# Performance work log

Measured on AMD Instinct MI355X. Metric: run time of the kernel, lower is better.

## Reference

```python
import jax, jax.numpy as jnp
import numpy as np

B, S, D = 8, 2048, 512          # batch, seq_len, latent_doc_dim
E = 512                          # embedding_dim (== latent_doc_dim here by construction)
NUM_CATS, NUM_LABELS = 1024, 8192
EMB_SCALING = 1.0


def _norm_embed(m, scaling):
    # __init__ preprocessing: m -= m.mean(); m /= m.std() * scaling
    m = m - m.mean()
    return m / (m.std() * scaling)


def setup_inputs() -> dict:
    key = jax.random.key(0)
    k1, k2, k3, k4, k5, k6, k7 = jax.random.split(key, 7)
    K = jax.random.normal(k1, (B, S, D), dtype=jnp.float32)
    V = jax.random.normal(k2, (B, S, D), dtype=jnp.float32)
    code2cat_map = jax.random.randint(k3, (NUM_LABELS,), 0, NUM_CATS)
    # pretrained embedding matrices, normalized as in __init__
    Q1_w = _norm_embed(jax.random.normal(k4, (NUM_CATS, E), dtype=jnp.float32), EMB_SCALING)
    Q2_w = _norm_embed(jax.random.normal(k5, (NUM_LABELS, E), dtype=jnp.float32), EMB_SCALING)
    # Conv1d(kernel_size=1): weight [D_out=latent, D_in=embed], bias [latent]
    map_w = jax.random.normal(k6, (D, E), dtype=jnp.float32) / np.sqrt(E)
    map_b = jax.random.normal(k7, (D,), dtype=jnp.float32) * 0.01
    return {"K": K, "V": V, "code2cat_map": code2cat_map,
            "Q1_w": Q1_w, "Q2_w": Q2_w, "map_w": map_w, "map_b": map_b}


def reference(K, V, code2cat_map, Q1_w, Q2_w, map_w, map_b):
    # kernel-size-1 Conv1d mapping == affine projection of each row embedding
    Q1 = jnp.einsum('ce,de->cd', Q1_w, map_w) + map_b        # [num_cats, D]
    Q2 = jnp.einsum('le,de->ld', Q2_w, map_w) + map_b        # [num_labels, D]
    # level-1 attention (scale=False)
    E1 = jnp.einsum('cd,bsd->bcs', Q1, K)                    # [B, num_cats, S]
    A1 = jax.nn.softmax(E1, axis=-1)
    C1 = jnp.einsum('bcs,bsd->bcd', A1, V)                   # [B, num_cats, D]
    # inject level-1 context into level-2 queries via code->category gather-add
    Q2b = Q2[None, :, :] + C1[:, code2cat_map, :]            # [B, num_labels, D]
    # level-2 attention
    E2 = jnp.einsum('bld,bsd->bls', Q2b, K)                  # [B, num_labels, S]
    A2 = jax.nn.softmax(E2, axis=-1)
    C2 = jnp.einsum('bls,bsd->bld', A2, V)                   # [B, num_labels, D]
    return (C2, E2)
```

## Files before the change

kernel.cpp:

```cpp
#include <hip/hip_runtime.h>
#include <hip/hip_bf16.h>
#include <stdint.h>

#define BB 8
#define SS 2048
#define DD 512
#define NCAT 1024
#define NLAB 8192

typedef short bf16x8 __attribute__((ext_vector_type(8)));
typedef short bf16x4_t __attribute__((ext_vector_type(4)));
typedef float f32x4 __attribute__((ext_vector_type(4)));

#define BAR() do { asm volatile("" ::: "memory"); __builtin_amdgcn_s_barrier(); asm volatile("" ::: "memory"); } while (0)

__device__ __forceinline__ unsigned short f2bf(float f) {
  union { float f; unsigned int u; } v; v.f = f;
  unsigned int u = v.u;
  return (unsigned short)((u + 0x7fffu + ((u >> 16) & 1u)) >> 16);
}
__device__ __forceinline__ float bf2f(unsigned short h) {
  union { unsigned int u; float f; } v; v.u = ((unsigned int)h) << 16;
  return v.f;
}

__device__ __forceinline__ void gload_lds16(const void* g, void* l) {
  __builtin_amdgcn_global_load_lds(
      (const __attribute__((address_space(1))) unsigned int*)g,
      (__attribute__((address_space(3))) unsigned int*)l, 16, 0, 0);
}

__global__ __launch_bounds__(512, 2) void gemm_qk512(
    const short* __restrict__ A, long sA,
    const short* __restrict__ Bc,
    float* __restrict__ E, float* __restrict__ pm, float* __restrict__ ps,
    int M)
{
  constexpr int NK = 16;
  __shared__ __align__(16) char lds[3 * 32768];
  const int t = threadIdx.x;
  const int w = t >> 6, lane = t & 63;
  const int r = lane & 15, g = lane >> 4;
  const int wm = w >> 2, wn = w & 3;
  const int m0 = blockIdx.x * 256, n0 = blockIdx.y * 256;
  const int b = blockIdx.z;
  const short* Ab = A + (long)b * sA;
  const short* Bb = Bc + (long)b * SS * DD;

  int offA[8], offB[4];
#pragma unroll
  for (int i = 0; i < 8; ++i) {
    int row = wm * 128 + i * 16 + r;
    int grp = row >> 1, slot = ((row & 1) << 2) | g;
    offA[i] = grp * 128 + (slot ^ (grp & 7)) * 16;
  }
#pragma unroll
  for (int j = 0; j < 4; ++j) {
    int row = wn * 64 + j * 16 + r;
    int grp = row >> 1, slot = ((row & 1) << 2) | g;
    offB[j] = grp * 128 + (slot ^ (grp & 7)) * 16;
  }

  int srow[2], scol[2];
#pragma unroll
  for (int ld = 0; ld < 2; ++ld) {
    int ch = ld * 512 + t;
    int grp = ch >> 3, sl2 = (ch & 7) ^ (grp & 7);
    srow[ld] = grp * 2 + (sl2 >> 2);
    scol[ld] = (sl2 & 3) * 8;
  }

  auto stageA = [&](int kt, int buf) {
    const long kb = (long)(kt * 32);
#pragma unroll
    for (int ld = 0; ld < 2; ++ld)
      gload_lds16(Ab + (long)(m0 + srow[ld]) * DD + kb + scol[ld],
                  lds + buf * 32768 + (ld * 512 + t) * 16);
  };
  auto stageB = [&](int kt, int buf) {
    const long kb = (long)(kt * 32);
#pragma unroll
    for (int ld = 0; ld < 2; ++ld)
      gload_lds16(Bb + (long)(n0 + srow[ld]) * DD + kb + scol[ld],
                  lds + buf * 32768 + 16384 + (ld * 512 + t) * 16);
  };

  f32x4 acc[8][4] = {};

  stageA(0, 0); stageB(0, 0);
  stageA(1, 1); stageB(1, 1);
  asm volatile("s_waitcnt vmcnt(4)" ::: "memory");
  BAR();

  int cur = 0;
#pragma unroll 1
  for (int kt = 0; kt < NK; ++kt) {
    const char* bA = lds + cur * 32768;
    const char* bB = bA + 16384;
    const int nxt = (cur == 0) ? 2 : cur - 1;

    bf16x8 av[4], av2[4], bv[4];
#pragma unroll
    for (int j = 0; j < 4; ++j) bv[j] = *(const bf16x8*)(bB + offB[j]);
#pragma unroll
    for (int i = 0; i < 4; ++i) av[i] = *(const bf16x8*)(bA + offA[i]);
    if (kt + 2 < NK) stageA(kt + 2, nxt);
    BAR();
    __builtin_amdgcn_s_setprio(1);
#pragma unroll
    for (int i = 0; i < 4; ++i)
#pragma unroll
      for (int j = 0; j < 4; ++j)
        acc[i][j] = __builtin_amdgcn_mfma_f32_16x16x32_bf16(av[i], bv[j], acc[i][j], 0, 0, 0);
    __builtin_amdgcn_s_setprio(0);
    BAR();
#pragma unroll
    for (int i = 0; i < 4; ++i) av2[i] = *(const bf16x8*)(bA + offA[4 + i]);
    if (kt + 2 < NK) stageB(kt + 2, nxt);
    BAR();
    __builtin_amdgcn_s_setprio(1);
#pragma unroll
    for (int i = 0; i < 4; ++i)
#pragma unroll
      for (int j = 0; j < 4; ++j)
        acc[4 + i][j] = __builtin_amdgcn_mfma_f32_16x16x32_bf16(av2[i], bv[j], acc[4 + i][j], 0, 0, 0);
    __builtin_amdgcn_s_setprio(0);
    if (kt < NK - 1) {
      if (kt == NK - 2) asm volatile("s_waitcnt vmcnt(0)" ::: "memory");
      else              asm volatile("s_waitcnt vmcnt(4)" ::: "memory");
    }
    BAR();
    cur = (cur == 2) ? 0 : cur + 1;
  }

  float* Cg = E + (long)b * M * SS;
#pragma unroll
  for (int i = 0; i < 8; ++i)
#pragma unroll
    for (int j = 0; j < 4; ++j) {
      const int col = n0 + wn * 64 + j * 16 + r;
#pragma unroll
      for (int q = 0; q < 4; ++q) {
        const int row = m0 + wm * 128 + i * 16 + g * 4 + q;
        Cg[(long)row * SS + col] = acc[i][j][q];
      }
    }

  BAR();

  float* smax = (float*)lds;
  float* ssum = (float*)(lds + 4096);
#pragma unroll
  for (int i = 0; i < 8; ++i)
#pragma unroll
    for (int q = 0; q < 4; ++q) {
      float mm = fmaxf(fmaxf(acc[i][0][q], acc[i][1][q]),
                       fmaxf(acc[i][2][q], acc[i][3][q]));
#pragma unroll
      for (int off = 1; off <= 8; off <<= 1) mm = fmaxf(mm, __shfl_xor(mm, off, 64));
      float s = 0.f;
#pragma unroll
      for (int j = 0; j < 4; ++j) s += __expf(acc[i][j][q] - mm);
#pragma unroll
      for (int off = 1; off <= 8; off <<= 1) s += __shfl_xor(s, off, 64);
      if (r == 0) {
        const int rowt = wm * 128 + i * 16 + g * 4 + q;
        smax[rowt * 4 + wn] = mm;
        ssum[rowt * 4 + wn] = s;
      }
    }
  BAR();
  if (t < 256) {
    float m0_ = smax[t * 4 + 0], m1_ = smax[t * 4 + 1];
    float m2_ = smax[t * 4 + 2], m3_ = smax[t * 4 + 3];
    float mm = fmaxf(fmaxf(m0_, m1_), fmaxf(m2_, m3_));
    float s = ssum[t * 4 + 0] * __expf(m0_ - mm) + ssum[t * 4 + 1] * __expf(m1_ - mm)
            + ssum[t * 4 + 2] * __expf(m2_ - mm) + ssum[t * 4 + 3] * __expf(m3_ - mm);
    const long base = ((long)b * M + m0 + t) * 8 + (n0 >> 8);
    pm[base] = mm;
    ps[base] = s;
  }
}

__global__ __launch_bounds__(512, 2) void gemm_pv(
    const float* __restrict__ E, const float2* __restrict__ stats,
    const short* __restrict__ VT, float* __restrict__ C, int M)
{
  __shared__ __align__(16) char lds[3 * 32768];
  const int t = threadIdx.x;
  const int w = t >> 6, lane = t & 63;
  const int r = lane & 15, g = lane >> 4;
  const int wm = w >> 2, wn = w & 3;
  const int m0 = blockIdx.x * 256, n0 = blockIdx.y * 256;
  const int b = blockIdx.z;
  const float* Eb = E + (long)b * M * SS;
  const short* Bb = VT + (long)b * DD * SS;

  int offA[8], offB[4];
#pragma unroll
  for (int i = 0; i < 8; ++i) {
    int row = wm * 128 + i * 16 + r;
    int grp = row >> 1, slot = ((row & 1) << 2) | g;
    offA[i] = grp * 128 + (slot ^ (grp & 7)) * 16;
  }
#pragma unroll
  for (int j = 0; j < 4; ++j) {
    int row = wn * 64 + j * 16 + r;
    int grp = row >> 1, slot = ((row & 1) << 2) | g;
    offB[j] = grp * 128 + (slot ^ (grp & 7)) * 16;
  }

  int srow[2], scol[2];
#pragma unroll
  for (int ld = 0; ld < 2; ++ld) {
    int ch = ld * 512 + t;
    int grp = ch >> 3, sl2 = (ch & 7) ^ (grp & 7);
    srow[ld] = grp * 2 + (sl2 >> 2);
    scol[ld] = (sl2 & 3) * 8;
  }

  const int arow = t >> 1;
  const int ac0 = (t & 1) * 16;
  int wbyte[2];
  {
    const int grp = arow >> 1, cc0 = ac0 >> 3;
#pragma unroll
    for (int ld = 0; ld < 2; ++ld) {
      const int slot = ((arow & 1) << 2) | (cc0 + ld);
      wbyte[ld] = grp * 128 + (slot ^ (grp & 7)) * 16;
    }
  }
  const float2 st = stats[(long)b * M + m0 + arow];
  const float* asrc = Eb + (long)(m0 + arow) * SS + ac0;

  float areg[16];
  auto loadA = [&](int kt) {
    const float* src = asrc + kt * 32;
#pragma unroll
    for (int u = 0; u < 4; ++u)
      *(f32x4*)(areg + u * 4) = *(const f32x4*)(src + u * 4);
  };
  auto writeA = [&](int buf) {
    char* dst = lds + buf * 32768;
#pragma unroll
    for (int ld = 0; ld < 2; ++ld) {
      bf16x8 p;
#pragma unroll
      for (int q = 0; q < 8; ++q)
        p[q] = (short)f2bf(__expf(areg[ld * 8 + q] - st.x) * st.y);
      *(bf16x8*)(dst + wbyte[ld]) = p;
    }
  };
  auto stageB = [&](int kt, int buf) {
    const long kb = (long)(kt * 32);
#pragma unroll
    for (int ld = 0; ld < 2; ++ld)
      gload_lds16(Bb + (long)(n0 + srow[ld]) * SS + kb + scol[ld],
                  lds + buf * 32768 + 16384 + (ld * 512 + t) * 16);
  };

  f32x4 acc[8][4] = {};

  loadA(0); stageB(0, 0); writeA(0);
  loadA(1); stageB(1, 1); writeA(1);
  asm volatile("s_waitcnt lgkmcnt(0)" ::: "memory");
  BAR();

  int cur = 0;
#pragma unroll 1
  for (int kt = 0; kt < 64; ++kt) {
    const char* bA = lds + cur * 32768;
    const char* bB = bA + 16384;
    const int nxt = (cur == 0) ? 2 : cur - 1;

    bf16x8 av[4], av2[4], bv[4];
#pragma unroll
    for (int j = 0; j < 4; ++j) bv[j] = *(const bf16x8*)(bB + offB[j]);
#pragma unroll
    for (int i = 0; i < 4; ++i) av[i] = *(const bf16x8*)(bA + offA[i]);
    if (kt + 2 < 64) loadA(kt + 2);
    BAR();
    __builtin_amdgcn_s_setprio(1);
#pragma unroll
    for (int i = 0; i < 4; ++i)
#pragma unroll
      for (int j = 0; j < 4; ++j)
        acc[i][j] = __builtin_amdgcn_mfma_f32_16x16x32_bf16(av[i], bv[j], acc[i][j], 0, 0, 0);
    __builtin_amdgcn_s_setprio(0);
    BAR();
#pragma unroll
    for (int i = 0; i < 4; ++i) av2[i] = *(const bf16x8*)(bA + offA[4 + i]);
    if (kt + 2 < 64) stageB(kt + 2, nxt);
    BAR();
    __builtin_amdgcn_s_setprio(1);
#pragma unroll
    for (int i = 0; i < 4; ++i)
#pragma unroll
      for (int j = 0; j < 4; ++j)
        acc[4 + i][j] = __builtin_amdgcn_mfma_f32_16x16x32_bf16(av2[i], bv[j], acc[4 + i][j], 0, 0, 0);
    __builtin_amdgcn_s_setprio(0);
    if (kt + 2 < 64) writeA(nxt);
    if (kt == 62) asm volatile("s_waitcnt vmcnt(0)" ::: "memory");
    asm volatile("s_waitcnt lgkmcnt(0)" ::: "memory");
    BAR();
    cur = (cur == 2) ? 0 : cur + 1;
  }

  float* Cg = C + (long)b * M * DD;
#pragma unroll
  for (int i = 0; i < 8; ++i)
#pragma unroll
    for (int j = 0; j < 4; ++j) {
      const int col = n0 + wn * 64 + j * 16 + r;
#pragma unroll
      for (int q = 0; q < 4; ++q) {
        const int row = m0 + wm * 128 + i * 16 + g * 4 + q;
        Cg[(long)row * DD + col] = acc[i][j][q];
      }
    }
}

template<int BIAS, int TERMS, int WQ>
__global__ __launch_bounds__(256) void gemm_nt_split(
    const short* __restrict__ Ah, const short* __restrict__ Al,
    const short* __restrict__ Bh, const short* __restrict__ Bl,
    float* __restrict__ C, short* __restrict__ Qph, short* __restrict__ Qpl,
    const float* __restrict__ bias,
    int M, int N, int K, long sA, long sB, long sC)
{
  __shared__ short AsH[128 * 32];
  __shared__ short AsL[TERMS == 3 ? 128 * 32 : 8];
  __shared__ short BsH[128 * 32];
  __shared__ short BsL[TERMS == 3 ? 128 * 32 : 8];
  const int t = threadIdx.x, w = t >> 6, l = t & 63;
  const int r = l & 15, g = l >> 4;
  const int m0 = blockIdx.x * 128, n0 = blockIdx.y * 128;
  const int b = blockIdx.z;
  const short* Ahb = Ah + (long)b * sA;
  const short* Alb = TERMS == 3 ? Al + (long)b * sA : (const short*)0;
  const short* Bhb = Bh + (long)b * sB;
  const short* Blb = TERMS == 3 ? Bl + (long)b * sB : (const short*)0;
  float* Cg = C + (long)b * sC;
  const int wm = (w >> 1) * 64, wn = (w & 1) * 64;
  const int srow = t >> 2, scol = (t & 3) * 8;

  f32x4 acc[4][4] = {};

  const int nk = K >> 5;
  for (int kt = 0; kt < nk; ++kt) {
    const long k0 = (long)(kt << 5);
    const long ga0 = (long)(m0 + srow) * K + k0 + scol;
    const long ga1 = (long)(m0 + srow + 64) * K + k0 + scol;
    const long gb0 = (long)(n0 + srow) * K + k0 + scol;
    const long gb1 = (long)(n0 + srow + 64) * K + k0 + scol;
    gload_lds16(Ahb + ga0, &AsH[w * 512]);
    gload_lds16(Ahb + ga1, &AsH[2048 + w * 512]);
    gload_lds16(Bhb + gb0, &BsH[w * 512]);
    gload_lds16(Bhb + gb1, &BsH[2048 + w * 512]);
    if (TERMS == 3) {
      gload_lds16(Alb + ga0, &AsL[w * 512]);
      gload_lds16(Alb + ga1, &AsL[2048 + w * 512]);
      gload_lds16(Blb + gb0, &BsL[w * 512]);
      gload_lds16(Blb + gb1, &BsL[2048 + w * 512]);
    }
    __syncthreads();
    bf16x8 ah[4], al_[4], bh[4], bl_[4];
#pragma unroll
    for (int i = 0; i < 4; ++i) {
      ah[i]  = *(const bf16x8*)&AsH[(wm + i * 16 + r) * 32 + g * 8];
      bh[i]  = *(const bf16x8*)&BsH[(wn + i * 16 + r) * 32 + g * 8];
      if (TERMS == 3) {
        al_[i] = *(const bf16x8*)&AsL[(wm + i * 16 + r) * 32 + g * 8];
        bl_[i] = *(const bf16x8*)&BsL[(wn + i * 16 + r) * 32 + g * 8];
      }
    }
#pragma unroll
    for (int i = 0; i < 4; ++i)
#pragma unroll
      for (int j = 0; j < 4; ++j) {
        if (TERMS == 3) {
          acc[i][j] = __builtin_amdgcn_mfma_f32_16x16x32_bf16(al_[i], bh[j], acc[i][j], 0, 0, 0);
          acc[i][j] = __builtin_amdgcn_mfma_f32_16x16x32_bf16(ah[i], bl_[j], acc[i][j], 0, 0, 0);
        }
        acc[i][j] = __builtin_amdgcn_mfma_f32_16x16x32_bf16(ah[i], bh[j], acc[i][j], 0, 0, 0);
      }
    __syncthreads();
  }

#pragma unroll
  for (int i = 0; i < 4; ++i)
#pragma unroll
    for (int j = 0; j < 4; ++j) {
      f32x4 v = acc[i][j];
      const int col = n0 + wn + j * 16 + r;
      float bv = 0.f;
      if (BIAS) bv = bias[col];
#pragma unroll
      for (int q = 0; q < 4; ++q) {
        const int row = m0 + wm + i * 16 + g * 4 + q;
        const float val = v[q] + bv;
        Cg[(long)row * N + col] = val;
        if (WQ && row < NCAT) {
          unsigned short h = f2bf(val);
          Qph[(long)row * N + col] = (short)h;
          Qpl[(long)row * N + col] = (short)f2bf(val - bf2f(h));
        }
      }
    }
}

__global__ __launch_bounds__(256) void stats_combine(
    const float* __restrict__ pm, const float* __restrict__ ps,
    float2* __restrict__ stats)
{
  const long row = (long)blockIdx.x * 256 + threadIdx.x;
  const float* m = pm + row * 8;
  const float* s = ps + row * 8;
  float mv[8];
  float mm = -3.4e38f;
#pragma unroll
  for (int j = 0; j < 8; ++j) { mv[j] = m[j]; mm = fmaxf(mm, mv[j]); }
  float ss = 0.f;
#pragma unroll
  for (int j = 0; j < 8; ++j) ss += s[j] * __expf(mv[j] - mm);
  stats[row] = make_float2(mm, 1.f / ss);
}

__global__ __launch_bounds__(256) void rowsoft_p(
    const float* __restrict__ X, short* __restrict__ Ph)
{
  __shared__ float red[8];
  const long row = blockIdx.x;
  const float* x = X + row * SS;
  const int t = threadIdx.x, w = t >> 6;
  f32x4 v0 = *(const f32x4*)(x + t * 4);
  f32x4 v1 = *(const f32x4*)(x + 1024 + t * 4);
  float m = fmaxf(fmaxf(fmaxf(v0[0], v0[1]), fmaxf(v0[2], v0[3])),
                  fmaxf(fmaxf(v1[0], v1[1]), fmaxf(v1[2], v1[3])));
#pragma unroll
  for (int off = 32; off; off >>= 1) m = fmaxf(m, __shfl_xor(m, off, 64));
  if ((t & 63) == 0) red[w] = m;
  __syncthreads();
  m = fmaxf(fmaxf(red[0], red[1]), fmaxf(red[2], red[3]));
  float s = 0.f;
#pragma unroll
  for (int i = 0; i < 4; ++i) { v0[i] = __expf(v0[i] - m); s += v0[i]; }
#pragma unroll
  for (int i = 0; i < 4; ++i) { v1[i] = __expf(v1[i] - m); s += v1[i]; }
#pragma unroll
  for (int off = 32; off; off >>= 1) s += __shfl_xor(s, off, 64);
  if ((t & 63) == 0) red[4 + w] = s;
  __syncthreads();
  s = red[4] + red[5] + red[6] + red[7];
  const float inv = 1.f / s;
  bf16x4_t h0, h1;
#pragma unroll
  for (int i = 0; i < 4; ++i) {
    h0[i] = (short)f2bf(v0[i] * inv);
    h1[i] = (short)f2bf(v1[i] * inv);
  }
  *(bf16x4_t*)(Ph + row * SS + t * 4) = h0;
  *(bf16x4_t*)(Ph + row * SS + 1024 + t * 4) = h1;
}

__global__ __launch_bounds__(256) void cvt_split(
    const float* __restrict__ in, short* __restrict__ hi, short* __restrict__ lo, long n4)
{
  long i = (long)blockIdx.x * 256 + threadIdx.x;
  const long stride = (long)gridDim.x * 256;
  for (; i < n4; i += stride) {
    f32x4 v = *(const f32x4*)(in + i * 4);
    bf16x4_t h, lw;
#pragma unroll
    for (int q = 0; q < 4; ++q) {
      h[q] = (short)f2bf(v[q]);
      lw[q] = (short)f2bf(v[q] - bf2f((unsigned short)h[q]));
    }
    *(bf16x4_t*)(hi + i * 4) = h;
    *(bf16x4_t*)(lo + i * 4) = lw;
  }
}

__global__ __launch_bounds__(256) void vtrans(
    const float* __restrict__ V, short* __restrict__ TH)
{
  __shared__ float tile[32][33];
  const int b = blockIdx.z;
  const int s0 = blockIdx.x * 32, d0 = blockIdx.y * 32;
  const int tx = threadIdx.x & 31, ty = threadIdx.x >> 5;
  const float* Vb = V + (long)b * SS * DD;
  short* Hb = TH + (long)b * DD * SS;
#pragma unroll
  for (int i = 0; i < 32; i += 8)
    tile[ty + i][tx] = Vb[(long)(s0 + ty + i) * DD + d0 + tx];
  __syncthreads();
#pragma unroll
  for (int i = 0; i < 32; i += 8)
    Hb[(long)(d0 + ty + i) * SS + s0 + tx] = (short)f2bf(tile[tx][ty + i]);
}

__global__ __launch_bounds__(256) void make_q2b(
    const float* __restrict__ Q2f, const float* __restrict__ C1,
    const int* __restrict__ map, short* __restrict__ Oh)
{
  const long idx = (long)blockIdx.x * 256 + threadIdx.x;
  const long per_b = (long)NLAB * (DD / 4);
  const int b = (int)(idx / per_b);
  const long rem = idx - (long)b * per_b;
  const int ll = (int)(rem >> 7);
  const int dd = (int)(rem & 127) << 2;
  const int cat = map[ll];
  f32x4 qv = *(const f32x4*)(Q2f + (long)ll * DD + dd);
  f32x4 cv = *(const f32x4*)(C1 + ((long)b * NCAT + cat) * DD + dd);
  bf16x4_t h;
#pragma unroll
  for (int q = 0; q < 4; ++q) h[q] = (short)f2bf(qv[q] + cv[q]);
  *(bf16x4_t*)(Oh + idx * 4) = h;
}

extern "C" void kernel_launch(void* const* d_in, const int* in_sizes, int n_in,
                              void* d_out, int out_size, void* d_ws, size_t ws_size,
                              hipStream_t stream)
{
  const float* K    = (const float*)d_in[0];
  const float* V    = (const float*)d_in[1];
  const int*   map  = (const int*)d_in[2];
  const float* Q1w  = (const float*)d_in[3];
  const float* Q2w  = (const float*)d_in[4];
  const float* mapw = (const float*)d_in[5];
  const float* mapb = (const float*)d_in[6];

  float* out = (float*)d_out;
  const long C2SZ = (long)BB * NLAB * DD;
  float* outC2 = out;
  float* outE2 = out + C2SZ;

  char* ws = (char*)d_ws;
  short* Kh    = (short*)ws; ws += (long)BB * SS * DD * 2;
  short* Kl    = (short*)ws; ws += (long)BB * SS * DD * 2;
  short* VTh   = (short*)ws; ws += (long)BB * DD * SS * 2;
  short* Qwh   = (short*)ws; ws += (long)(NCAT + NLAB) * DD * 2;
  short* Qwl   = (short*)ws; ws += (long)(NCAT + NLAB) * DD * 2;
  short* mwh   = (short*)ws; ws += (long)DD * DD * 2;
  short* mwl   = (short*)ws; ws += (long)DD * DD * 2;
  float* Qall  = (float*)ws; ws += (long)(NCAT + NLAB) * DD * 4;
  short* Qph   = (short*)ws; ws += (long)NCAT * DD * 2;
  short* Qpl   = (short*)ws; ws += (long)NCAT * DD * 2;
  short* A1h   = (short*)ws; ws += (long)BB * NCAT * SS * 2;
  float* C1    = (float*)ws; ws += (long)BB * NCAT * DD * 4;
  short* Q2bh  = (short*)ws; ws += (long)BB * NLAB * DD * 2;
  float* pm    = (float*)ws; ws += (long)BB * NLAB * 8 * 4;
  float* psum  = (float*)ws; ws += (long)BB * NLAB * 8 * 4;
  float2* stats = (float2*)ws;

  cvt_split<<<2048, 256, 0, stream>>>(K, Kh, Kl, (long)BB * SS * DD / 4);
  vtrans<<<dim3(SS / 32, DD / 32, BB), 256, 0, stream>>>(V, VTh);
  cvt_split<<<512, 256, 0, stream>>>(Q1w, Qwh, Qwl, (long)NCAT * DD / 4);
  cvt_split<<<2048, 256, 0, stream>>>(Q2w, Qwh + (long)NCAT * DD, Qwl + (long)NCAT * DD,
                                      (long)NLAB * DD / 4);
  cvt_split<<<256, 256, 0, stream>>>(mapw, mwh, mwl, (long)DD * DD / 4);

  gemm_nt_split<1, 3, 1><<<dim3((NCAT + NLAB) / 128, DD / 128, 1), 256, 0, stream>>>(
      Qwh, Qwl, mwh, mwl, Qall, Qph, Qpl, mapb, NCAT + NLAB, DD, DD, 0, 0, 0);

  gemm_nt_split<0, 3, 0><<<dim3(NCAT / 128, SS / 128, BB), 256, 0, stream>>>(
      Qph, Qpl, Kh, Kl, outE2, (short*)0, (short*)0, (const float*)0,
      NCAT, SS, DD, 0, (long)SS * DD, (long)NCAT * SS);

  rowsoft_p<<<BB * NCAT, 256, 0, stream>>>(outE2, A1h);

  gemm_nt_split<0, 1, 0><<<dim3(NCAT / 128, DD / 128, BB), 256, 0, stream>>>(
      A1h, (const short*)0, VTh, (const short*)0, C1, (short*)0, (short*)0,
      (const float*)0, NCAT, DD, SS, (long)NCAT * SS, (long)DD * SS, (long)NCAT * DD);

  make_q2b<<<(int)((long)BB * NLAB * DD / 4 / 256), 256, 0, stream>>>(
      Qall + (long)NCAT * DD, C1, map, Q2bh);

  gemm_qk512<<<dim3(NLAB / 256, SS / 256, BB), 512, 0, stream>>>(
      Q2bh, (long)NLAB * DD, Kh, outE2, pm, psum, NLAB);
  stats_combine<<<BB * NLAB / 256, 256, 0, stream>>>(pm, psum, stats);

  gemm_pv<<<dim3(NLAB / 256, DD / 256, BB), 512, 0, stream>>>(
      outE2, stats, VTh, outC2, NLAB);
}
```

Before: 787.9 us.

## Fuse level-1 softmax into QK epilogue and PV prologue, drop rowsoft pass

Level-1 softmax row statistics (partial max and sum) are now computed in the epilogue of the Q1·K GEMM and combined by a small stats kernel. A new PV GEMM reads raw fp32 logits and applies exp-normalize-to-bf16 while staging A into LDS. This removes the separate row-softmax kernel and the bf16 A1 intermediate, saving a full read and write pass over the B×1024×2048 scores. In exchange, the PV kernel now reads fp32 logits (twice the bytes of bf16) through synchronous register loads with exp work in the main loop, which may limit overlap.

```diff
diff --git a/kernel.cpp b/kernel.cpp
--- a/kernel.cpp
+++ b/kernel.cpp
@@ -320,18 +320,84 @@
     }
 }
 
-template<int BIAS, int TERMS, int WQ>
+__global__ __launch_bounds__(256) void gemm_pv128(
+    const float* __restrict__ E, const float2* __restrict__ stats,
+    const short* __restrict__ VT, float* __restrict__ C, int M)
+{
+  __shared__ short As[128 * 32];
+  __shared__ short Bs[128 * 32];
+  const int t = threadIdx.x, w = t >> 6, l = t & 63;
+  const int r = l & 15, g = l >> 4;
+  const int m0 = blockIdx.x * 128, n0 = blockIdx.y * 128;
+  const int b = blockIdx.z;
+  const float* Eb = E + (long)b * M * SS;
+  const short* Bb = VT + (long)b * DD * SS;
+  float* Cg = C + (long)b * M * DD;
+  const int wm = (w >> 1) * 64, wn = (w & 1) * 64;
+  const int srow = t >> 2, scol = (t & 3) * 8;
+
+  const int arow = t >> 1, ac0 = (t & 1) * 16;
+  const float2 st = stats[(long)b * M + m0 + arow];
+  const float* asrc = Eb + (long)(m0 + arow) * SS + ac0;
+
+  f32x4 acc[4][4] = {};
+
+  for (int kt = 0; kt < (SS >> 5); ++kt) {
+    const int k0 = kt << 5;
+    gload_lds16(Bb + (long)(n0 + srow) * SS + k0 + scol, &Bs[w * 512]);
+    gload_lds16(Bb + (long)(n0 + srow + 64) * SS + k0 + scol, &Bs[2048 + w * 512]);
+    float areg[16];
+#pragma unroll
+    for (int u = 0; u < 4; ++u)
+      *(f32x4*)(areg + u * 4) = *(const f32x4*)(asrc + k0 + u * 4);
+    bf16x8 p0, p1;
+#pragma unroll
+    for (int q = 0; q < 8; ++q) p0[q] = (short)f2bf(__expf(areg[q] - st.x) * st.y);
+#pragma unroll
+    for (int q = 0; q < 8; ++q) p1[q] = (short)f2bf(__expf(areg[8 + q] - st.x) * st.y);
+    *(bf16x8*)&As[arow * 32 + ac0] = p0;
+    *(bf16x8*)&As[arow * 32 + ac0 + 8] = p1;
+    __syncthreads();
+    bf16x8 af[4], bfr[4];
+#pragma unroll
+    for (int i = 0; i < 4; ++i) {
+      af[i]  = *(const bf16x8*)&As[(wm + i * 16 + r) * 32 + g * 8];
+      bfr[i] = *(const bf16x8*)&Bs[(wn + i * 16 + r) * 32 + g * 8];
+    }
+#pragma unroll
+    for (int i = 0; i < 4; ++i)
+#pragma unroll
+      for (int j = 0; j < 4; ++j)
+        acc[i][j] = __builtin_amdgcn_mfma_f32_16x16x32_bf16(af[i], bfr[j], acc[i][j], 0, 0, 0);
+    __syncthreads();
+  }
+
+#pragma unroll
+  for (int i = 0; i < 4; ++i)
+#pragma unroll
+    for (int j = 0; j < 4; ++j) {
+      f32x4 v = acc[i][j];
+      const int col = n0 + wn + j * 16 + r;
+#pragma unroll
+      for (int q = 0; q < 4; ++q)
+        Cg[(long)(m0 + wm + i * 16 + g * 4 + q) * DD + col] = v[q];
+    }
+}
+
+template<int BIAS, int TERMS, int WQ, int STATS>
 __global__ __launch_bounds__(256) void gemm_nt_split(
     const short* __restrict__ Ah, const short* __restrict__ Al,
     const short* __restrict__ Bh, const short* __restrict__ Bl,
     float* __restrict__ C, short* __restrict__ Qph, short* __restrict__ Qpl,
-    const float* __restrict__ bias,
+    const float* __restrict__ bias, float* __restrict__ pm, float* __restrict__ ps,
     int M, int N, int K, long sA, long sB, long sC)
 {
   __shared__ short AsH[128 * 32];
   __shared__ short AsL[TERMS == 3 ? 128 * 32 : 8];
   __shared__ short BsH[128 * 32];
   __shared__ short BsL[TERMS == 3 ? 128 * 32 : 8];
+  __shared__ float smax[STATS ? 256 : 4];
+  __shared__ float ssum[STATS ? 256 : 4];
   const int t = threadIdx.x, w = t >> 6, l = t & 63;
   const int r = l & 15, g = l >> 4;
   const int m0 = blockIdx.x * 128, n0 = blockIdx.y * 128;
@@ -407,60 +473,57 @@
         }
       }
     }
-}
-
+
+  if (STATS) {
+#pragma unroll
+    for (int i = 0; i < 4; ++i)
+#pragma unroll
+      for (int q = 0; q < 4; ++q) {
+        float mm = fmaxf(fmaxf(acc[i][0][q], acc[i][1][q]),
+                         fmaxf(acc[i][2][q], acc[i][3][q]));
+#pragma unroll
+        for (int off = 1; off <= 8; off <<= 1) mm = fmaxf(mm, __shfl_xor(mm, off, 64));
+        float s = 0.f;
+#pragma unroll
+        for (int j = 0; j < 4; ++j) s += __expf(acc[i][j][q] - mm);
+#pragma unroll
+        for (int off = 1; off <= 8; off <<= 1) s += __shfl_xor(s, off, 64);
+        if (r == 0) {
+          const int rl = i * 16 + g * 4 + q;
+          smax[w * 64 + rl] = mm;
+          ssum[w * 64 + rl] = s;
+        }
+      }
+    __syncthreads();
+    if ((w & 1) == 0) {
+      const float m0_ = smax[w * 64 + l], m1_ = smax[(w + 1) * 64 + l];
+      const float s0_ = ssum[w * 64 + l], s1_ = ssum[(w + 1) * 64 + l];
+      const float mm = fmaxf(m0_, m1_);
+      const float s = s0_ * __expf(m0_ - mm) + s1_ * __expf(m1_ - mm);
+      const int row = m0 + (w >> 1) * 64 + l;
+      const long base = ((long)b * M + row) * (long)(N >> 7) + (n0 >> 7);
+      pm[base] = mm;
+      ps[base] = s;
+    }
+  }
+}
+
+template<int NP>
 __global__ __launch_bounds__(256) void stats_combine(
     const float* __restrict__ pm, const float* __restrict__ ps,
     float2* __restrict__ stats)
 {
   const long row = (long)blockIdx.x * 256 + threadIdx.x;
-  const float* m = pm + row * 8;
-  const float* s = ps + row * 8;
-  float mv[8];
+  const float* m = pm + row * NP;
+  const float* s = ps + row * NP;
+  float mv[NP];
   float mm = -3.4e38f;
 #pragma unroll
-  for (int j = 0; j < 8; ++j) { mv[j] = m[j]; mm = fmaxf(mm, mv[j]); }
+  for (int j = 0; j < NP; ++j) { mv[j] = m[j]; mm = fmaxf(mm, mv[j]); }
   float ss = 0.f;
 #pragma unroll
-  for (int j = 0; j < 8; ++j) ss += s[j] * __expf(mv[j] - mm);
+  for (int j = 0; j < NP; ++j) ss += s[j] * __expf(mv[j] - mm);
   stats[row] = make_float2(mm, 1.f / ss);
-}
-
-__global__ __launch_bounds__(256) void rowsoft_p(
-    const float* __restrict__ X, short* __restrict__ Ph)
-{
-  __shared__ float red[8];
-  const long row = blockIdx.x;
-  const float* x = X + row * SS;
-  const int t = threadIdx.x, w = t >> 6;
-  f32x4 v0 = *(const f32x4*)(x + t * 4);
-  f32x4 v1 = *(const f32x4*)(x + 1024 + t * 4);
-  float m = fmaxf(fmaxf(fmaxf(v0[0], v0[1]), fmaxf(v0[2], v0[3])),
-                  fmaxf(fmaxf(v1[0], v1[1]), fmaxf(v1[2], v1[3])));
-#pragma unroll
-  for (int off = 32; off; off >>= 1) m = fmaxf(m, __shfl_xor(m, off, 64));
-  if ((t & 63) == 0) red[w] = m;
-  __syncthreads();
-  m = fmaxf(fmaxf(red[0], red[1]), fmaxf(red[2], red[3]));
-  float s = 0.f;
-#pragma unroll
-  for (int i = 0; i < 4; ++i) { v0[i] = __expf(v0[i] - m); s += v0[i]; }
-#pragma unroll
-  for (int i = 0; i < 4; ++i) { v1[i] = __expf(v1[i] - m); s += v1[i]; }
-#pragma unroll
-  for (int off = 32; off; off >>= 1) s += __shfl_xor(s, off, 64);
-  if ((t & 63) == 0) red[4 + w] = s;
-  __syncthreads();
-  s = red[4] + red[5] + red[6] + red[7];
-  const float inv = 1.f / s;
-  bf16x4_t h0, h1;
-#pragma unroll
-  for (int i = 0; i < 4; ++i) {
-    h0[i] = (short)f2bf(v0[i] * inv);
-    h1[i] = (short)f2bf(v1[i] * inv);
-  }
-  *(bf16x4_t*)(Ph + row * SS + t * 4) = h0;
-  *(bf16x4_t*)(Ph + row * SS + 1024 + t * 4) = h1;
 }
 
 __global__ __launch_bounds__(256) void cvt_split(
@@ -546,12 +609,14 @@
   float* Qall  = (float*)ws; ws += (long)(NCAT + NLAB) * DD * 4;
   short* Qph   = (short*)ws; ws += (long)NCAT * DD * 2;
   short* Qpl   = (short*)ws; ws += (long)NCAT * DD * 2;
-  short* A1h   = (short*)ws; ws += (long)BB * NCAT * SS * 2;
   float* C1    = (float*)ws; ws += (long)BB * NCAT * DD * 4;
   short* Q2bh  = (short*)ws; ws += (long)BB * NLAB * DD * 2;
   float* pm    = (float*)ws; ws += (long)BB * NLAB * 8 * 4;
   float* psum  = (float*)ws; ws += (long)BB * NLAB * 8 * 4;
-  float2* stats = (float2*)ws;
+  float* pm1   = (float*)ws; ws += (long)BB * NCAT * 16 * 4;
+  float* ps1   = (float*)ws; ws += (long)BB * NCAT * 16 * 4;
+  float2* stats  = (float2*)ws; ws += (long)BB * NLAB * 8;
+  float2* stats1 = (float2*)ws;
 
   cvt_split<<<2048, 256, 0, stream>>>(K, Kh, Kl, (long)BB * SS * DD / 4);
   vtrans<<<dim3(SS / 32, DD / 32, BB), 256, 0, stream>>>(V, VTh);
@@ -560,25 +625,24 @@
                                       (long)NLAB * DD / 4);
   cvt_split<<<256, 256, 0, stream>>>(mapw, mwh, mwl, (long)DD * DD / 4);
 
-  gemm_nt_split<1, 3, 1><<<dim3((NCAT + NLAB) / 128, DD / 128, 1), 256, 0, stream>>>(
-      Qwh, Qwl, mwh, mwl, Qall, Qph, Qpl, mapb, NCAT + NLAB, DD, DD, 0, 0, 0);
-
-  gemm_nt_split<0, 3, 0><<<dim3(NCAT / 128, SS / 128, BB), 256, 0, stream>>>(
-      Qph, Qpl, Kh, Kl, outE2, (short*)0, (short*)0, (const float*)0,
+  gemm_nt_split<1, 3, 1, 0><<<dim3((NCAT + NLAB) / 128, DD / 128, 1), 256, 0, stream>>>(
+      Qwh, Qwl, mwh, mwl, Qall, Qph, Qpl, mapb, (float*)0, (float*)0,
+      NCAT + NLAB, DD, DD, 0, 0, 0);
+
+  gemm_nt_split<0, 3, 0, 1><<<dim3(NCAT / 128, SS / 128, BB), 256, 0, stream>>>(
+      Qph, Qpl, Kh, Kl, outE2, (short*)0, (short*)0, (const float*)0, pm1, ps1,
       NCAT, SS, DD, 0, (long)SS * DD, (long)NCAT * SS);
-
-  rowsoft_p<<<BB * NCAT, 256, 0, stream>>>(outE2, A1h);
-
-  gemm_nt_split<0, 1, 0><<<dim3(NCAT / 128, DD / 128, BB), 256, 0, stream>>>(
-      A1h, (const short*)0, VTh, (const short*)0, C1, (short*)0, (short*)0,
-      (const float*)0, NCAT, DD, SS, (long)NCAT * SS, (long)DD * SS, (long)NCAT * DD);
+  stats_combine<16><<<BB * NCAT / 256, 256, 0, stream>>>(pm1, ps1, stats1);
+
+  gemm_pv128<<<dim3(NCAT / 128, DD / 128, BB), 256, 0, stream>>>(
+      outE2, stats1, VTh, C1, NCAT);
 
   make_q2b<<<(int)((long)BB * NLAB * DD / 4 / 256), 256, 0, stream>>>(
       Qall + (long)NCAT * DD, C1, map, Q2bh);
 
   gemm_qk512<<<dim3(NLAB / 256, SS / 256, BB), 512, 0, stream>>>(
       Q2bh, (long)NLAB * DD, Kh, outE2, pm, psum, NLAB);
-  stats_combine<<<BB * NLAB / 256, 256, 0, stream>>>(pm, psum, stats);
+  stats_combine<8><<<BB * NLAB / 256, 256, 0, stream>>>(pm, psum, stats);
 
   gemm_pv<<<dim3(NLAB / 256, DD / 256, BB), 512, 0, stream>>>(
       outE2, stats, VTh, outC2, NLAB);
```

After: 819.9 us. 1.04x slower.
